# Optimization experiments

Measured on AMD Instinct MI355X. Metric: run time of the kernel, lower is better.

The kernel has to match this reference:

```python
import jax, jax.numpy as jnp
import numpy as np
from jax import lax

SCORE_THRESH = 0.05
NMS_THRESH = 0.5
DET_PER_IMG = 100
WX, WY, WW, WH = 10.0, 10.0, 5.0, 5.0   # BoxCoder weights
BBOX_XFORM_CLIP = float(np.log(1000.0 / 16.0))
NEG = -1e9  # sentinel for invalid / suppressed scores


def setup_inputs() -> dict:
    key = jax.random.key(0)
    k1, k2, k3 = jax.random.split(key, 3)
    R, C = 1000, 81
    W, H = 1333, 800
    class_logits = jax.random.normal(k1, (R, C), dtype=jnp.float32)
    box_regression = jax.random.normal(k2, (R, C * 4), dtype=jnp.float32)
    # build valid xyxy proposal boxes inside the image from uniform noise
    u = jax.random.uniform(k3, (R, 4), dtype=jnp.float32)
    x1 = u[:, 0] * (W - 120)
    y1 = u[:, 1] * (H - 120)
    x2 = jnp.minimum(x1 + 20.0 + u[:, 2] * 300.0, W - 1)
    y2 = jnp.minimum(y1 + 20.0 + u[:, 3] * 300.0, H - 1)
    proposals = jnp.stack([x1, y1, x2, y2], axis=1)
    return {"class_logits": class_logits, "box_regression": box_regression,
            "proposals": proposals, "image_w": W, "image_h": H}


def _decode(rel, boxes):
    """BoxCoder.decode: rel [R, C*4], boxes [R,4] xyxy -> [R, C, 4]."""
    w = boxes[:, 2] - boxes[:, 0] + 1.0
    h = boxes[:, 3] - boxes[:, 1] + 1.0
    cx = boxes[:, 0] + 0.5 * w
    cy = boxes[:, 1] + 0.5 * h
    dx = rel[:, 0::4] / WX
    dy = rel[:, 1::4] / WY
    dw = jnp.minimum(rel[:, 2::4] / WW, BBOX_XFORM_CLIP)
    dh = jnp.minimum(rel[:, 3::4] / WH, BBOX_XFORM_CLIP)
    pcx = dx * w[:, None] + cx[:, None]
    pcy = dy * h[:, None] + cy[:, None]
    pw = jnp.exp(dw) * w[:, None]
    ph = jnp.exp(dh) * h[:, None]
    return jnp.stack([pcx - 0.5 * pw, pcy - 0.5 * ph,
                      pcx + 0.5 * pw - 1.0, pcy + 0.5 * ph - 1.0], axis=-1)


def _pairwise_iou(b):
    """Legacy (+1) IoU: b [N,4] -> [N,N]."""
    area = (b[:, 2] - b[:, 0] + 1.0) * (b[:, 3] - b[:, 1] + 1.0)
    lt = jnp.maximum(b[:, None, :2], b[None, :, :2])
    rb = jnp.minimum(b[:, None, 2:], b[None, :, 2:])
    wh = jnp.clip(rb - lt + 1.0, 0.0)
    inter = wh[..., 0] * wh[..., 1]
    return inter / (area[:, None] + area[None, :] - inter)


def _nms_one_class(boxes, scores):
    """Greedy NMS for one class, fixed shape. Returns keep mask [N] in original order."""
    N = scores.shape[0]
    valid = scores > SCORE_THRESH
    order = jnp.argsort(-jnp.where(valid, scores, NEG))
    b = boxes[order]
    v = valid[order]
    iou = _pairwise_iou(b)  # [N,N], descending-score order
    idx = jnp.arange(N)

    def body(keep, xs):
        i, row, vi = xs
        suppressed = jnp.any(keep & (row > NMS_THRESH) & (idx < i))
        keep = keep.at[i].set(vi & jnp.logical_not(suppressed))
        return keep, None

    keep_sorted, _ = lax.scan(body, jnp.zeros(N, bool), (idx, iou, v))
    return jnp.zeros(N, bool).at[order].set(keep_sorted)


def _forward(class_logits, box_regression, proposals, image_w, image_h):
    probs = jax.nn.softmax(class_logits, axis=-1)          # [R, C]
    boxes = _decode(box_regression, proposals)             # [R, C, 4]
    # clip_to_image (remove_empty=False), legacy -1 convention
    x = jnp.clip(boxes[..., 0::2], 0.0, image_w - 1)
    y = jnp.clip(boxes[..., 1::2], 0.0, image_h - 1)
    boxes = jnp.stack([x[..., 0], y[..., 0], x[..., 1], y[..., 1]], axis=-1)
    # drop background class 0
    sc = probs[:, 1:].T                                    # [C-1, R]
    bc = jnp.transpose(boxes[:, 1:, :], (1, 0, 2))         # [C-1, R, 4]
    keep = jax.vmap(_nms_one_class)(bc, sc)                # [C-1, R]
    flat_s = jnp.where(keep, sc, NEG).reshape(-1)
    top_s, top_i = lax.top_k(flat_s, DET_PER_IMG)
    top_b = bc.reshape(-1, 4)[top_i]
    labels = top_i // sc.shape[1] + 1
    return top_s, top_b, labels


def reference(class_logits, box_regression, proposals, image_w, image_h):
    return _forward(class_logits, box_regression, proposals, image_w, image_h)
```

## Files before the change

kernel.cpp:

```cpp
#include <hip/hip_runtime.h>
#include <cmath>

#define R_ROWS 1000
#define NCLS   81
#define REGW   (NCLS * 4)
#define SCORE_T 0.05f
#define NMS_T   0.5f
#define NEG_S  -1e9f
#define DETS   100
#define CLIP_V 4.135166556742356f
#define MAXC   1000
#define SLOTS  1000
#define NBLK_CLS 80

#define NBINS    1024
#define CK_CAP   2560
#define SURV_CAP 512


__device__ __forceinline__ float4 decode_clip(const float* __restrict__ prop,
                                              const float* __restrict__ reg,
                                              int r, int ccol, float wmax, float hmax) {
    float x1 = prop[r * 4 + 0], y1 = prop[r * 4 + 1];
    float x2 = prop[r * 4 + 2], y2 = prop[r * 4 + 3];
    float w  = __fadd_rn(__fsub_rn(x2, x1), 1.0f);
    float h  = __fadd_rn(__fsub_rn(y2, y1), 1.0f);
    float cx = __fadd_rn(x1, __fmul_rn(0.5f, w));
    float cy = __fadd_rn(y1, __fmul_rn(0.5f, h));
    const float* rr = reg + r * REGW + 4 * ccol;
    float dx = rr[0] / 10.0f;
    float dy = rr[1] / 10.0f;
    float dw = fminf(rr[2] / 5.0f, CLIP_V);
    float dh = fminf(rr[3] / 5.0f, CLIP_V);
    float pcx = __fadd_rn(__fmul_rn(dx, w), cx);
    float pcy = __fadd_rn(__fmul_rn(dy, h), cy);
    float pw  = __fmul_rn(expf(dw), w);
    float ph  = __fmul_rn(expf(dh), h);
    float ox1 = __fsub_rn(pcx, __fmul_rn(0.5f, pw));
    float oy1 = __fsub_rn(pcy, __fmul_rn(0.5f, ph));
    float ox2 = __fsub_rn(__fadd_rn(pcx, __fmul_rn(0.5f, pw)), 1.0f);
    float oy2 = __fsub_rn(__fadd_rn(pcy, __fmul_rn(0.5f, ph)), 1.0f);
    float4 o;
    o.x = fminf(fmaxf(ox1, 0.0f), wmax);
    o.y = fminf(fmaxf(oy1, 0.0f), hmax);
    o.z = fminf(fmaxf(ox2, 0.0f), wmax);
    o.w = fminf(fmaxf(oy2, 0.0f), hmax);
    return o;
}

__device__ __forceinline__ float iou_legacy(float ax1, float ay1, float ax2, float ay2,
                                            float bx1, float by1, float bx2, float by2) {
    float aw = __fadd_rn(__fsub_rn(ax2, ax1), 1.0f);
    float ah = __fadd_rn(__fsub_rn(ay2, ay1), 1.0f);
    float areaA = __fmul_rn(aw, ah);
    float bw = __fadd_rn(__fsub_rn(bx2, bx1), 1.0f);
    float bh = __fadd_rn(__fsub_rn(by2, by1), 1.0f);
    float areaB = __fmul_rn(bw, bh);
    float ltx = fmaxf(ax1, bx1), lty = fmaxf(ay1, by1);
    float rbx = fminf(ax2, bx2), rby = fminf(ay2, by2);
    float wx = fmaxf(__fadd_rn(__fsub_rn(rbx, ltx), 1.0f), 0.0f);
    float wy = fmaxf(__fadd_rn(__fsub_rn(rby, lty), 1.0f), 0.0f);
    float inter = __fmul_rn(wx, wy);
    float denom = __fsub_rn(__fadd_rn(areaA, areaB), inter);
    return inter / denom;
}

__device__ __forceinline__ int bin_of(float s) {
    int idx = (int)(__float_as_uint(s) >> 16) - 0x3D00;
    return idx < 0 ? 0 : (idx > NBINS - 1 ? NBINS - 1 : idx);
}

__device__ __forceinline__ unsigned long long key_of(float s, unsigned f) {
    return ((unsigned long long)__float_as_uint(s) << 32) | (unsigned long long)(~f);
}
__device__ __forceinline__ float key_score(unsigned long long k) {
    return __uint_as_float((unsigned)(k >> 32));
}
__device__ __forceinline__ int key_flat(unsigned long long k) {
    return (int)(~(unsigned)k);
}

__device__ __forceinline__ void dev_store_u64(unsigned long long* p, unsigned long long v) {
    __hip_atomic_store(p, v, __ATOMIC_RELAXED, __HIP_MEMORY_SCOPE_AGENT);
}
__device__ __forceinline__ unsigned long long dev_load_u64(const unsigned long long* p) {
    return __hip_atomic_load(p, __ATOMIC_RELAXED, __HIP_MEMORY_SCOPE_AGENT);
}
__device__ __forceinline__ void dev_store_i32(int* p, int v) {
    __hip_atomic_store(p, v, __ATOMIC_RELAXED, __HIP_MEMORY_SCOPE_AGENT);
}

__device__ __forceinline__ int find_class(const int* koff, int g) {
    int lo = 0, hi = NBLK_CLS;
    while (hi - lo > 1) { int mid = (lo + hi) >> 1; if (g >= koff[mid]) lo = mid; else hi = mid; }
    return lo;
}


__global__ __launch_bounds__(64) void k_softmax_stats(const float* __restrict__ logits,
                                                      float* __restrict__ rowmax,
                                                      float* __restrict__ rowsum,
                                                      int* __restrict__ done) {
    int r = blockIdx.x;
    int l = threadIdx.x;
    if (r == 0 && l == 0) *done = 0;
    float v1 = logits[r * NCLS + l];
    float v2 = (l < NCLS - 64) ? logits[r * NCLS + 64 + l] : -INFINITY;
    float m = fmaxf(v1, v2);
    #pragma unroll
    for (int off = 32; off; off >>= 1) m = fmaxf(m, __shfl_xor(m, off));
    float s = expf(__fsub_rn(v1, m));
    if (l < NCLS - 64) s = __fadd_rn(s, expf(__fsub_rn(v2, m)));
    #pragma unroll
    for (int off = 32; off; off >>= 1) s = __fadd_rn(s, __shfl_xor(s, off));
    if (l == 0) { rowmax[r] = m; rowsum[r] = s; }
}


__global__ __launch_bounds__(256) void k_nms_select(const float* __restrict__ logits,
                                                    const float* __restrict__ reg,
                                                    const float* __restrict__ prop,
                                                    const float* __restrict__ rowmax,
                                                    const float* __restrict__ rowsum,
                                                    const int* __restrict__ piw,
                                                    const int* __restrict__ pih,
                                                    unsigned long long* __restrict__ klist,
                                                    int* __restrict__ kcount,
                                                    int* __restrict__ done,
                                                    float* __restrict__ out) {
    __shared__ float us[MAXC];  __shared__ int uidx[MAXC];
    __shared__ float ss[MAXC];  __shared__ int sidx[MAXC];
    __shared__ float bx4[MAXC][4];
    __shared__ int   supp[MAXC];
    __shared__ int   cnt, sh_last;
    __shared__ int   koff[NBLK_CLS + 1];
    __shared__ int   cs[256];
    __shared__ int   hist_s[NBINS];
    __shared__ unsigned long long ck[CK_CAP + 4];
    __shared__ unsigned long long cks[SURV_CAP + 4];
    __shared__ float sel_s[DETS]; __shared__ int sel_f[DETS];
    __shared__ int   sh_cut, sh_mcnt;

    const int cidx = blockIdx.x;
    const int ccol = cidx + 1;
    const int t    = threadIdx.x;
    const int lane = t & 63;
    const int wv   = t >> 6;
    const float wmax = (float)(*piw - 1);
    const float hmax = (float)(*pih - 1);

    if (t == 0) cnt = 0;
    __syncthreads();

    for (int r = t; r < R_ROWS; r += 256) {
        float z = logits[r * NCLS + ccol];
        float s = expf(__fsub_rn(z, rowmax[r])) / rowsum[r];
        if (s > SCORE_T) {
            int p = atomicAdd(&cnt, 1);
            us[p] = s; uidx[p] = r;
        }
    }
    __syncthreads();
    const int M = cnt;

    for (int i = t; i < M; i += 256) {
        float si = us[i]; int ri = uidx[i];
        int rank = 0;
        for (int j = 0; j < M; j++) {
            float sj = us[j]; int rj = uidx[j];
            rank += (sj > si) || (sj == si && rj < ri);
        }
        ss[rank] = si; sidx[rank] = ri;
    }
    __syncthreads();
    for (int i = t; i < M; i += 256) {
        float4 b = decode_clip(prop, reg, sidx[i], ccol, wmax, hmax);
        bx4[i][0] = b.x; bx4[i][1] = b.y; bx4[i][2] = b.z; bx4[i][3] = b.w;
        supp[i] = 0;
    }
    __syncthreads();

    if (M <= 64) {
        if (wv == 0) {
            const bool valid = lane < M;
            float b0 = 0, b1 = 0, b2 = 0, b3 = 0, sc = 0; int ri = 0;
            if (valid) { b0 = bx4[lane][0]; b1 = bx4[lane][1]; b2 = bx4[lane][2]; b3 = bx4[lane][3];
                         sc = ss[lane]; ri = sidx[lane]; }
            unsigned long long suppm = 0;
            for (int i = 0; i < M; ++i) {
                if ((suppm >> i) & 1ULL) continue;
                float ax1 = __shfl(b0, i), ay1 = __shfl(b1, i);
                float ax2 = __shfl(b2, i), ay2 = __shfl(b3, i);
                bool kill = valid && (lane > i) &&
                            (iou_legacy(ax1, ay1, ax2, ay2, b0, b1, b2, b3) > NMS_T);
                suppm |= __ballot(kill);
            }
            unsigned long long keepm = ~suppm;
            if (M < 64) keepm &= (1ULL << M) - 1ULL;
            if (valid && ((keepm >> lane) & 1ULL)) {
                int pos = __popcll(keepm & ((1ULL << lane) - 1ULL));
                dev_store_u64(&klist[(size_t)cidx * SLOTS + pos],
                              key_of(sc, (unsigned)(cidx * R_ROWS + ri)));
            }
            if (lane == 0) dev_store_i32(&kcount[cidx], __popcll(keepm));
        }
    } else {
        for (int i = 0; i < M; i++) {
            if (!supp[i]) {
                float ax1 = bx4[i][0], ay1 = bx4[i][1], ax2 = bx4[i][2], ay2 = bx4[i][3];
                for (int j = i + 1 + t; j < M; j += 256) {
                    if (!supp[j]) {
                        float v = iou_legacy(ax1, ay1, ax2, ay2,
                                             bx4[j][0], bx4[j][1], bx4[j][2], bx4[j][3]);
                        if (v > NMS_T) supp[j] = 1;
                    }
                }
            }
            __syncthreads();
        }
        for (int i = t; i < M; i += 256) {
            if (!supp[i]) {
                int pos = 0;
                for (int j = 0; j < i; ++j) pos += !supp[j];
                dev_store_u64(&klist[(size_t)cidx * SLOTS + pos],
                              key_of(ss[i], (unsigned)(cidx * R_ROWS + sidx[i])));
            }
        }
        if (t == 0) {
            int kc = 0;
            for (int i = 0; i < M; ++i) kc += !supp[i];
            dev_store_i32(&kcount[cidx], kc);
        }
    }

    __syncthreads();
    if (t == 0) sh_last = (atomicAdd(done, 1) == NBLK_CLS - 1) ? 1 : 0;
    __syncthreads();
    if (!sh_last) return;

    if (t < NBLK_CLS) cs[t] = atomicAdd(&kcount[t], 0);
    for (int b = t; b < NBINS; b += 256) hist_s[b] = 0;
    __syncthreads();
    if (t == 0) {
        int acc = 0;
        for (int c = 0; c < NBLK_CLS; ++c) { koff[c] = acc; acc += cs[c]; }
        koff[NBLK_CLS] = acc;
        sh_cut = 0; sh_mcnt = 0;
    }
    __syncthreads();
    const int K = koff[NBLK_CLS];
    const int target = (K < DETS) ? K : DETS;

    if (K <= CK_CAP) {
        for (int g = t; g < K; g += 256) {
            int c = find_class(koff, g);
            unsigned long long k = dev_load_u64(&klist[(size_t)c * SLOTS + (g - koff[c])]);
            ck[g] = k;
            atomicAdd(&hist_s[bin_of(key_score(k))], 1);
        }
        __syncthreads();

        int v0 = hist_s[4 * t], v1 = hist_s[4 * t + 1], v2 = hist_s[4 * t + 2], v3 = hist_s[4 * t + 3];
        int s3 = v3, s2 = v2 + s3, s1 = v1 + s2, s0 = v0 + s1;
        cs[t] = s0;
        __syncthreads();
        for (int off = 1; off < 256; off <<= 1) {
            int x = cs[t] + ((t + off < 256) ? cs[t + off] : 0);
            __syncthreads();
            cs[t] = x;
            __syncthreads();
        }
        int tail = (t < 255) ? cs[t + 1] : 0;
        int S0 = s0 + tail, S1 = s1 + tail, S2 = s2 + tail, S3 = s3 + tail;
        if (target > 0) {
            int best = -1;
            if      (S3 >= target) best = 4 * t + 3;
            else if (S2 >= target) best = 4 * t + 2;
            else if (S1 >= target) best = 4 * t + 1;
            else if (S0 >= target) best = 4 * t;
            if (best >= 0) atomicMax(&sh_cut, best);
        }
        __syncthreads();
        const int cut = sh_cut;

        for (int g = t; g < K; g += 256) {
            unsigned long long k = ck[g];
            if (bin_of(key_score(k)) >= cut) {
                int p = atomicAdd(&sh_mcnt, 1);
                if (p < SURV_CAP) cks[p] = k;
            }
        }
        __syncthreads();
        const int Mc = sh_mcnt;

        if (Mc <= SURV_CAP) {
            int Mp = (Mc + 3) & ~3;
            if (t < Mp - Mc) cks[Mc + t] = 0;
            __syncthreads();
            for (int i = t; i < Mc; i += 256) {
                unsigned long long ki = cks[i];
                int r = 0;
                for (int j = 0; j < Mp; j += 4)
                    r += (int)(cks[j] > ki) + (int)(cks[j + 1] > ki)
                       + (int)(cks[j + 2] > ki) + (int)(cks[j + 3] > ki);
                if (r < DETS) {
                    sel_s[r] = key_score(ki);
                    sel_f[r] = key_flat(ki);
                }
            }
        } else {
            int Kp = (K + 3) & ~3;
            if (t < Kp - K) ck[K + t] = 0;
            __syncthreads();
            for (int g = t; g < K; g += 256) {
                unsigned long long ki = ck[g];
                if (bin_of(key_score(ki)) < cut) continue;
                int r = 0;
                for (int j = 0; j < Kp; j += 4)
                    r += (int)(ck[j] > ki) + (int)(ck[j + 1] > ki)
                       + (int)(ck[j + 2] > ki) + (int)(ck[j + 3] > ki);
                if (r < DETS) {
                    sel_s[r] = key_score(ki);
                    sel_f[r] = key_flat(ki);
                }
            }
        }
    } else {
        for (int g = t; g < K; g += 256) {
            int c = find_class(koff, g);
            unsigned long long ki = dev_load_u64(&klist[(size_t)c * SLOTS + (g - koff[c])]);
            int r = 0;
            for (int g2 = 0; g2 < K; ++g2) {
                int c2 = find_class(koff, g2);
                r += (int)(dev_load_u64(&klist[(size_t)c2 * SLOTS + (g2 - koff[c2])]) > ki);
            }
            if (r < DETS) {
                sel_s[r] = key_score(ki);
                sel_f[r] = key_flat(ki);
            }
        }
    }
    __syncthreads();

    if (t == 0 && target < DETS) {
        int n = target, f = 0;
        while (n < DETS) {
            bool used = false;
            for (int q = 0; q < target; q++) if (key_flat(cks[q]) == f) { used = true; break; }
            if (!used) { sel_s[n] = NEG_S; sel_f[n] = f; n++; }
            f++;
        }
    }
    __syncthreads();

    if (t < DETS) {
        int f = sel_f[t];
        int c2 = f / R_ROWS;
        int r  = f % R_ROWS;
        float4 b = decode_clip(prop, reg, r, c2 + 1, wmax, hmax);
        out[t] = sel_s[t];
        out[DETS + 4 * t + 0] = b.x;
        out[DETS + 4 * t + 1] = b.y;
        out[DETS + 4 * t + 2] = b.z;
        out[DETS + 4 * t + 3] = b.w;
        out[DETS * 5 + t] = (float)(c2 + 1);
    }
}


extern "C" void kernel_launch(void* const* d_in, const int* in_sizes, int n_in,
                              void* d_out, int out_size, void* d_ws, size_t ws_size,
                              hipStream_t stream) {
    (void)in_sizes; (void)n_in; (void)out_size; (void)ws_size;
    const float* logits = (const float*)d_in[0];
    const float* reg    = (const float*)d_in[1];
    const float* prop   = (const float*)d_in[2];
    const int*   piw    = (const int*)d_in[3];
    const int*   pih    = (const int*)d_in[4];
    float* out = (float*)d_out;

    char* ws = (char*)d_ws;
    int*   done    = (int*)(ws);
    int*   kcount  = (int*)(ws + 64);
    float* rowmax  = (float*)(ws + 1024);
    float* rowsum  = (float*)(ws + 5120);
    unsigned long long* klist = (unsigned long long*)(ws + 12288);

    k_softmax_stats<<<dim3(R_ROWS), dim3(64), 0, stream>>>(logits, rowmax, rowsum, done);
    k_nms_select<<<dim3(NBLK_CLS), dim3(256), 0, stream>>>(logits, reg, prop, rowmax, rowsum,
                                                           piw, pih, klist, kcount, done, out);
}
```

Baseline: 38.32 us.

## Fuse softmax stats into NMS kernel with chunked LDS logits staging

Removes the separate softmax-stats kernel. Each of the 80 class blocks now recomputes the row max and sum for all 1000 rows, staging the logits through shared memory in 128-row chunks. Shared buffers are overlaid in one union region to make room for the staging area, and the done flag is reset with a memset. This saves a kernel launch and the global round trip for the stats, but every block redundantly reads the full logits matrix and does a serial 81-element softmax per thread, using only 128 of its 256 threads.

```diff
diff --git a/kernel.cpp b/kernel.cpp
--- a/kernel.cpp
+++ b/kernel.cpp
@@ -12,6 +12,9 @@
 #define MAXC   1000
 #define SLOTS  1000
 #define NBLK_CLS 80
+
+#define CHUNK_R 128
+#define NCHUNK  8
 
 #define NBINS    1024
 #define CK_CAP   2560
@@ -97,49 +100,30 @@
 }
 
 
-__global__ __launch_bounds__(64) void k_softmax_stats(const float* __restrict__ logits,
-                                                      float* __restrict__ rowmax,
-                                                      float* __restrict__ rowsum,
-                                                      int* __restrict__ done) {
-    int r = blockIdx.x;
-    int l = threadIdx.x;
-    if (r == 0 && l == 0) *done = 0;
-    float v1 = logits[r * NCLS + l];
-    float v2 = (l < NCLS - 64) ? logits[r * NCLS + 64 + l] : -INFINITY;
-    float m = fmaxf(v1, v2);
-    #pragma unroll
-    for (int off = 32; off; off >>= 1) m = fmaxf(m, __shfl_xor(m, off));
-    float s = expf(__fsub_rn(v1, m));
-    if (l < NCLS - 64) s = __fadd_rn(s, expf(__fsub_rn(v2, m)));
-    #pragma unroll
-    for (int off = 32; off; off >>= 1) s = __fadd_rn(s, __shfl_xor(s, off));
-    if (l == 0) { rowmax[r] = m; rowsum[r] = s; }
-}
-
-
-__global__ __launch_bounds__(256) void k_nms_select(const float* __restrict__ logits,
-                                                    const float* __restrict__ reg,
-                                                    const float* __restrict__ prop,
-                                                    const float* __restrict__ rowmax,
-                                                    const float* __restrict__ rowsum,
-                                                    const int* __restrict__ piw,
-                                                    const int* __restrict__ pih,
-                                                    unsigned long long* __restrict__ klist,
-                                                    int* __restrict__ kcount,
-                                                    int* __restrict__ done,
-                                                    float* __restrict__ out) {
+__global__ __launch_bounds__(256) void k_all(const float* __restrict__ logits,
+                                             const float* __restrict__ reg,
+                                             const float* __restrict__ prop,
+                                             const int* __restrict__ piw,
+                                             const int* __restrict__ pih,
+                                             unsigned long long* __restrict__ klist,
+                                             int* __restrict__ kcount,
+                                             int* __restrict__ done,
+                                             float* __restrict__ out) {
     __shared__ float us[MAXC];  __shared__ int uidx[MAXC];
-    __shared__ float ss[MAXC];  __shared__ int sidx[MAXC];
-    __shared__ float bx4[MAXC][4];
-    __shared__ int   supp[MAXC];
-    __shared__ int   cnt, sh_last;
+    __shared__ int cnt, sh_last;
     __shared__ int   koff[NBLK_CLS + 1];
     __shared__ int   cs[256];
-    __shared__ int   hist_s[NBINS];
-    __shared__ unsigned long long ck[CK_CAP + 4];
-    __shared__ unsigned long long cks[SURV_CAP + 4];
     __shared__ float sel_s[DETS]; __shared__ int sel_f[DETS];
     __shared__ int   sh_cut, sh_mcnt;
+    __shared__ __align__(16) char ubuf[41472];
+    float* chunkf = (float*)ubuf;
+    float* ss   = (float*)ubuf;
+    int*   sidx = (int*)(ubuf + 4000);
+    float (*bx4)[4] = (float(*)[4])(ubuf + 8000);
+    int*   supp = (int*)(ubuf + 24000);
+    int*   hist_s = (int*)ubuf;
+    unsigned long long* ck  = (unsigned long long*)(ubuf + 4096);
+    unsigned long long* cks = (unsigned long long*)(ubuf + 4096 + 8 * CK_CAP);
 
     const int cidx = blockIdx.x;
     const int ccol = cidx + 1;
@@ -152,15 +136,30 @@
     if (t == 0) cnt = 0;
     __syncthreads();
 
-    for (int r = t; r < R_ROWS; r += 256) {
-        float z = logits[r * NCLS + ccol];
-        float s = expf(__fsub_rn(z, rowmax[r])) / rowsum[r];
-        if (s > SCORE_T) {
-            int p = atomicAdd(&cnt, 1);
-            us[p] = s; uidx[p] = r;
-        }
-    }
-    __syncthreads();
+    for (int c = 0; c < NCHUNK; ++c) {
+        const int rb = c * CHUNK_R;
+        int n = R_ROWS - rb; if (n > CHUNK_R) n = CHUNK_R;
+        const int nw = n * NCLS;
+        const float4* src = (const float4*)(logits + rb * NCLS);
+        float4* dst = (float4*)chunkf;
+        for (int i = t; i < (nw >> 2); i += 256) dst[i] = src[i];
+        __syncthreads();
+        if (t < n) {
+            const float* row = chunkf + t * NCLS;
+            float m = row[0];
+            #pragma unroll 8
+            for (int k = 1; k < NCLS; ++k) m = fmaxf(m, row[k]);
+            float s = 0.0f;
+            #pragma unroll 8
+            for (int k = 0; k < NCLS; ++k) s = __fadd_rn(s, expf(__fsub_rn(row[k], m)));
+            float sc = expf(__fsub_rn(row[ccol], m)) / s;
+            if (sc > SCORE_T) {
+                int p = atomicAdd(&cnt, 1);
+                us[p] = sc; uidx[p] = rb + t;
+            }
+        }
+        __syncthreads();
+    }
     const int M = cnt;
 
     for (int i = t; i < M; i += 256) {
@@ -382,11 +381,9 @@
     char* ws = (char*)d_ws;
     int*   done    = (int*)(ws);
     int*   kcount  = (int*)(ws + 64);
-    float* rowmax  = (float*)(ws + 1024);
-    float* rowsum  = (float*)(ws + 5120);
-    unsigned long long* klist = (unsigned long long*)(ws + 12288);
-
-    k_softmax_stats<<<dim3(R_ROWS), dim3(64), 0, stream>>>(logits, rowmax, rowsum, done);
-    k_nms_select<<<dim3(NBLK_CLS), dim3(256), 0, stream>>>(logits, reg, prop, rowmax, rowsum,
-                                                           piw, pih, klist, kcount, done, out);
-}
+    unsigned long long* klist = (unsigned long long*)(ws + 4096);
+
+    hipMemsetAsync(ws, 0, 4, stream);
+    k_all<<<dim3(NBLK_CLS), dim3(256), 0, stream>>>(logits, reg, prop, piw, pih,
+                                                    klist, kcount, done, out);
+}
```

Result: slower. 102.5 us (+167.4%).

## Split last-block-done selection into a separate single-block kernel launch

Applied to the files above, without the earlier changes.

The per-class NMS kernel no longer uses an atomic done counter to elect a final block for global top-k selection. Selection now runs in its own one-block kernel, with the kernel boundary providing ordering, so plain loads and stores replace the agent-scope atomics. This shrinks the NMS kernel's shared memory, which may raise occupancy, and removes the atomic handoff. In exchange it adds a third kernel launch and its launch gap to the critical path.

```diff
diff --git a/kernel.cpp b/kernel.cpp
--- a/kernel.cpp
+++ b/kernel.cpp
@@ -80,16 +80,6 @@
     return (int)(~(unsigned)k);
 }
 
-__device__ __forceinline__ void dev_store_u64(unsigned long long* p, unsigned long long v) {
-    __hip_atomic_store(p, v, __ATOMIC_RELAXED, __HIP_MEMORY_SCOPE_AGENT);
-}
-__device__ __forceinline__ unsigned long long dev_load_u64(const unsigned long long* p) {
-    return __hip_atomic_load(p, __ATOMIC_RELAXED, __HIP_MEMORY_SCOPE_AGENT);
-}
-__device__ __forceinline__ void dev_store_i32(int* p, int v) {
-    __hip_atomic_store(p, v, __ATOMIC_RELAXED, __HIP_MEMORY_SCOPE_AGENT);
-}
-
 __device__ __forceinline__ int find_class(const int* koff, int g) {
     int lo = 0, hi = NBLK_CLS;
     while (hi - lo > 1) { int mid = (lo + hi) >> 1; if (g >= koff[mid]) lo = mid; else hi = mid; }
@@ -97,13 +87,11 @@
 }
 
 
-__global__ __launch_bounds__(64) void k_softmax_stats(const float* __restrict__ logits,
-                                                      float* __restrict__ rowmax,
-                                                      float* __restrict__ rowsum,
-                                                      int* __restrict__ done) {
+__global__ __launch_bounds__(64) void k_stats(const float* __restrict__ logits,
+                                              float* __restrict__ rowmax,
+                                              float* __restrict__ rowsum) {
     int r = blockIdx.x;
     int l = threadIdx.x;
-    if (r == 0 && l == 0) *done = 0;
     float v1 = logits[r * NCLS + l];
     float v2 = (l < NCLS - 64) ? logits[r * NCLS + 64 + l] : -INFINITY;
     float m = fmaxf(v1, v2);
@@ -117,29 +105,20 @@
 }
 
 
-__global__ __launch_bounds__(256) void k_nms_select(const float* __restrict__ logits,
-                                                    const float* __restrict__ reg,
-                                                    const float* __restrict__ prop,
-                                                    const float* __restrict__ rowmax,
-                                                    const float* __restrict__ rowsum,
-                                                    const int* __restrict__ piw,
-                                                    const int* __restrict__ pih,
-                                                    unsigned long long* __restrict__ klist,
-                                                    int* __restrict__ kcount,
-                                                    int* __restrict__ done,
-                                                    float* __restrict__ out) {
+__global__ __launch_bounds__(256) void k_nms(const float* __restrict__ logits,
+                                             const float* __restrict__ reg,
+                                             const float* __restrict__ prop,
+                                             const float* __restrict__ rowmax,
+                                             const float* __restrict__ rowsum,
+                                             const int* __restrict__ piw,
+                                             const int* __restrict__ pih,
+                                             unsigned long long* __restrict__ klist,
+                                             int* __restrict__ kcount) {
     __shared__ float us[MAXC];  __shared__ int uidx[MAXC];
     __shared__ float ss[MAXC];  __shared__ int sidx[MAXC];
     __shared__ float bx4[MAXC][4];
     __shared__ int   supp[MAXC];
-    __shared__ int   cnt, sh_last;
-    __shared__ int   koff[NBLK_CLS + 1];
-    __shared__ int   cs[256];
-    __shared__ int   hist_s[NBINS];
-    __shared__ unsigned long long ck[CK_CAP + 4];
-    __shared__ unsigned long long cks[SURV_CAP + 4];
-    __shared__ float sel_s[DETS]; __shared__ int sel_f[DETS];
-    __shared__ int   sh_cut, sh_mcnt;
+    __shared__ int   cnt;
 
     const int cidx = blockIdx.x;
     const int ccol = cidx + 1;
@@ -199,10 +178,9 @@
             if (M < 64) keepm &= (1ULL << M) - 1ULL;
             if (valid && ((keepm >> lane) & 1ULL)) {
                 int pos = __popcll(keepm & ((1ULL << lane) - 1ULL));
-                dev_store_u64(&klist[(size_t)cidx * SLOTS + pos],
-                              key_of(sc, (unsigned)(cidx * R_ROWS + ri)));
-            }
-            if (lane == 0) dev_store_i32(&kcount[cidx], __popcll(keepm));
+                klist[(size_t)cidx * SLOTS + pos] = key_of(sc, (unsigned)(cidx * R_ROWS + ri));
+            }
+            if (lane == 0) kcount[cidx] = __popcll(keepm);
         }
     } else {
         for (int i = 0; i < M; i++) {
@@ -222,23 +200,38 @@
             if (!supp[i]) {
                 int pos = 0;
                 for (int j = 0; j < i; ++j) pos += !supp[j];
-                dev_store_u64(&klist[(size_t)cidx * SLOTS + pos],
-                              key_of(ss[i], (unsigned)(cidx * R_ROWS + sidx[i])));
+                klist[(size_t)cidx * SLOTS + pos] = key_of(ss[i], (unsigned)(cidx * R_ROWS + sidx[i]));
             }
         }
         if (t == 0) {
             int kc = 0;
             for (int i = 0; i < M; ++i) kc += !supp[i];
-            dev_store_i32(&kcount[cidx], kc);
-        }
-    }
-
-    __syncthreads();
-    if (t == 0) sh_last = (atomicAdd(done, 1) == NBLK_CLS - 1) ? 1 : 0;
-    __syncthreads();
-    if (!sh_last) return;
-
-    if (t < NBLK_CLS) cs[t] = atomicAdd(&kcount[t], 0);
+            kcount[cidx] = kc;
+        }
+    }
+}
+
+
+__global__ __launch_bounds__(256) void k_select(const float* __restrict__ reg,
+                                                const float* __restrict__ prop,
+                                                const int* __restrict__ piw,
+                                                const int* __restrict__ pih,
+                                                const unsigned long long* __restrict__ klist,
+                                                const int* __restrict__ kcount,
+                                                float* __restrict__ out) {
+    __shared__ int   koff[NBLK_CLS + 1];
+    __shared__ int   cs[256];
+    __shared__ int   hist_s[NBINS];
+    __shared__ unsigned long long ck[CK_CAP + 4];
+    __shared__ unsigned long long cks[SURV_CAP + 4];
+    __shared__ float sel_s[DETS]; __shared__ int sel_f[DETS];
+    __shared__ int   sh_cut, sh_mcnt;
+
+    const int t = threadIdx.x;
+    const float wmax = (float)(*piw - 1);
+    const float hmax = (float)(*pih - 1);
+
+    if (t < NBLK_CLS) cs[t] = kcount[t];
     for (int b = t; b < NBINS; b += 256) hist_s[b] = 0;
     __syncthreads();
     if (t == 0) {
@@ -254,7 +247,7 @@
     if (K <= CK_CAP) {
         for (int g = t; g < K; g += 256) {
             int c = find_class(koff, g);
-            unsigned long long k = dev_load_u64(&klist[(size_t)c * SLOTS + (g - koff[c])]);
+            unsigned long long k = klist[(size_t)c * SLOTS + (g - koff[c])];
             ck[g] = k;
             atomicAdd(&hist_s[bin_of(key_score(k))], 1);
         }
@@ -328,11 +321,11 @@
     } else {
         for (int g = t; g < K; g += 256) {
             int c = find_class(koff, g);
-            unsigned long long ki = dev_load_u64(&klist[(size_t)c * SLOTS + (g - koff[c])]);
+            unsigned long long ki = klist[(size_t)c * SLOTS + (g - koff[c])];
             int r = 0;
             for (int g2 = 0; g2 < K; ++g2) {
                 int c2 = find_class(koff, g2);
-                r += (int)(dev_load_u64(&klist[(size_t)c2 * SLOTS + (g2 - koff[c2])]) > ki);
+                r += (int)(klist[(size_t)c2 * SLOTS + (g2 - koff[c2])] > ki);
             }
             if (r < DETS) {
                 sel_s[r] = key_score(ki);
@@ -380,13 +373,13 @@
     float* out = (float*)d_out;
 
     char* ws = (char*)d_ws;
-    int*   done    = (int*)(ws);
-    int*   kcount  = (int*)(ws + 64);
+    int*   kcount  = (int*)(ws);
     float* rowmax  = (float*)(ws + 1024);
     float* rowsum  = (float*)(ws + 5120);
     unsigned long long* klist = (unsigned long long*)(ws + 12288);
 
-    k_softmax_stats<<<dim3(R_ROWS), dim3(64), 0, stream>>>(logits, rowmax, rowsum, done);
-    k_nms_select<<<dim3(NBLK_CLS), dim3(256), 0, stream>>>(logits, reg, prop, rowmax, rowsum,
-                                                           piw, pih, klist, kcount, done, out);
-}
+    k_stats<<<dim3(R_ROWS), dim3(64), 0, stream>>>(logits, rowmax, rowsum);
+    k_nms<<<dim3(NBLK_CLS), dim3(256), 0, stream>>>(logits, reg, prop, rowmax, rowsum,
+                                                    piw, pih, klist, kcount);
+    k_select<<<dim3(1), dim3(256), 0, stream>>>(reg, prop, piw, pih, klist, kcount, out);
+}
```

After: 38.83 us. No clear change (+1.3%).

## Emit thresholded score keys in softmax kernel; NMS reads compacted per-class lists

Applied to the files above, without the earlier changes.

The softmax stats kernel now computes the per-class probabilities itself and appends packed (score, index) keys above threshold into per-class global lists via atomics. The NMS kernel no longer rescans all 1000 logits per class; it loads the compacted list and ranks with single 64-bit key compares. A memset is added to zero the counters, and the emit order is nondeterministic, which the full-key rank sort makes harmless. This trades a redundant per-class pass for global atomics and an extra memset launch.

```diff
diff --git a/kernel.cpp b/kernel.cpp
--- a/kernel.cpp
+++ b/kernel.cpp
@@ -9,13 +9,14 @@
 #define NEG_S  -1e9f
 #define DETS   100
 #define CLIP_V 4.135166556742356f
-#define MAXC   1000
 #define SLOTS  1000
 #define NBLK_CLS 80
 
 #define NBINS    1024
 #define CK_CAP   2560
 #define SURV_CAP 512
+
+typedef unsigned long long ull;
 
 
 __device__ __forceinline__ float4 decode_clip(const float* __restrict__ prop,
@@ -70,20 +71,16 @@
     return idx < 0 ? 0 : (idx > NBINS - 1 ? NBINS - 1 : idx);
 }
 
-__device__ __forceinline__ unsigned long long key_of(float s, unsigned f) {
-    return ((unsigned long long)__float_as_uint(s) << 32) | (unsigned long long)(~f);
-}
-__device__ __forceinline__ float key_score(unsigned long long k) {
-    return __uint_as_float((unsigned)(k >> 32));
-}
-__device__ __forceinline__ int key_flat(unsigned long long k) {
-    return (int)(~(unsigned)k);
-}
-
-__device__ __forceinline__ void dev_store_u64(unsigned long long* p, unsigned long long v) {
+__device__ __forceinline__ ull key_of(float s, unsigned f) {
+    return ((ull)__float_as_uint(s) << 32) | (ull)(~f);
+}
+__device__ __forceinline__ float key_score(ull k) { return __uint_as_float((unsigned)(k >> 32)); }
+__device__ __forceinline__ int   key_flat(ull k)  { return (int)(~(unsigned)k); }
+
+__device__ __forceinline__ void dev_store_u64(ull* p, ull v) {
     __hip_atomic_store(p, v, __ATOMIC_RELAXED, __HIP_MEMORY_SCOPE_AGENT);
 }
-__device__ __forceinline__ unsigned long long dev_load_u64(const unsigned long long* p) {
+__device__ __forceinline__ ull dev_load_u64(const ull* p) {
     return __hip_atomic_load(p, __ATOMIC_RELAXED, __HIP_MEMORY_SCOPE_AGENT);
 }
 __device__ __forceinline__ void dev_store_i32(int* p, int v) {
@@ -97,13 +94,11 @@
 }
 
 
-__global__ __launch_bounds__(64) void k_softmax_stats(const float* __restrict__ logits,
-                                                      float* __restrict__ rowmax,
-                                                      float* __restrict__ rowsum,
-                                                      int* __restrict__ done) {
+__global__ __launch_bounds__(64) void k_stats_emit(const float* __restrict__ logits,
+                                                   int* __restrict__ cnt,
+                                                   ull* __restrict__ klistA) {
     int r = blockIdx.x;
     int l = threadIdx.x;
-    if (r == 0 && l == 0) *done = 0;
     float v1 = logits[r * NCLS + l];
     float v2 = (l < NCLS - 64) ? logits[r * NCLS + 64 + l] : -INFINITY;
     float m = fmaxf(v1, v2);
@@ -113,31 +108,45 @@
     if (l < NCLS - 64) s = __fadd_rn(s, expf(__fsub_rn(v2, m)));
     #pragma unroll
     for (int off = 32; off; off >>= 1) s = __fadd_rn(s, __shfl_xor(s, off));
-    if (l == 0) { rowmax[r] = m; rowsum[r] = s; }
-}
-
-
-__global__ __launch_bounds__(256) void k_nms_select(const float* __restrict__ logits,
-                                                    const float* __restrict__ reg,
+
+    if (l >= 1) {
+        float sc = expf(__fsub_rn(v1, m)) / s;
+        if (sc > SCORE_T) {
+            int p = atomicAdd(&cnt[l], 1);
+            klistA[(size_t)(l - 1) * SLOTS + p] = key_of(sc, (unsigned)((l - 1) * R_ROWS + r));
+        }
+    }
+    if (l < NCLS - 64) {
+        int c = 64 + l;
+        float sc = expf(__fsub_rn(v2, m)) / s;
+        if (sc > SCORE_T) {
+            int p = atomicAdd(&cnt[c], 1);
+            klistA[(size_t)(c - 1) * SLOTS + p] = key_of(sc, (unsigned)((c - 1) * R_ROWS + r));
+        }
+    }
+}
+
+
+__global__ __launch_bounds__(256) void k_nms_select(const float* __restrict__ reg,
                                                     const float* __restrict__ prop,
-                                                    const float* __restrict__ rowmax,
-                                                    const float* __restrict__ rowsum,
                                                     const int* __restrict__ piw,
                                                     const int* __restrict__ pih,
-                                                    unsigned long long* __restrict__ klist,
+                                                    const int* __restrict__ cnt,
+                                                    const ull* __restrict__ klistA,
+                                                    ull* __restrict__ klistB,
                                                     int* __restrict__ kcount,
                                                     int* __restrict__ done,
                                                     float* __restrict__ out) {
-    __shared__ float us[MAXC];  __shared__ int uidx[MAXC];
-    __shared__ float ss[MAXC];  __shared__ int sidx[MAXC];
-    __shared__ float bx4[MAXC][4];
-    __shared__ int   supp[MAXC];
-    __shared__ int   cnt, sh_last;
+    __shared__ ull ku[SLOTS];
+    __shared__ ull ks[SLOTS];
+    __shared__ float bx4[SLOTS][4];
+    __shared__ int   supp[SLOTS];
+    __shared__ int   sh_last;
     __shared__ int   koff[NBLK_CLS + 1];
     __shared__ int   cs[256];
     __shared__ int   hist_s[NBINS];
-    __shared__ unsigned long long ck[CK_CAP + 4];
-    __shared__ unsigned long long cks[SURV_CAP + 4];
+    __shared__ ull   ck[CK_CAP + 4];
+    __shared__ ull   cks[SURV_CAP + 4];
     __shared__ float sel_s[DETS]; __shared__ int sel_f[DETS];
     __shared__ int   sh_cut, sh_mcnt;
 
@@ -149,32 +158,22 @@
     const float wmax = (float)(*piw - 1);
     const float hmax = (float)(*pih - 1);
 
-    if (t == 0) cnt = 0;
-    __syncthreads();
-
-    for (int r = t; r < R_ROWS; r += 256) {
-        float z = logits[r * NCLS + ccol];
-        float s = expf(__fsub_rn(z, rowmax[r])) / rowsum[r];
-        if (s > SCORE_T) {
-            int p = atomicAdd(&cnt, 1);
-            us[p] = s; uidx[p] = r;
-        }
-    }
-    __syncthreads();
-    const int M = cnt;
+    int M = cnt[ccol]; if (M > SLOTS) M = SLOTS;
+
+    for (int i = t; i < M; i += 256) ku[i] = klistA[(size_t)cidx * SLOTS + i];
+    __syncthreads();
 
     for (int i = t; i < M; i += 256) {
-        float si = us[i]; int ri = uidx[i];
+        ull ki = ku[i];
         int rank = 0;
-        for (int j = 0; j < M; j++) {
-            float sj = us[j]; int rj = uidx[j];
-            rank += (sj > si) || (sj == si && rj < ri);
-        }
-        ss[rank] = si; sidx[rank] = ri;
-    }
-    __syncthreads();
+        for (int j = 0; j < M; j++) rank += (int)(ku[j] > ki);
+        ks[rank] = ki;
+    }
+    __syncthreads();
+
     for (int i = t; i < M; i += 256) {
-        float4 b = decode_clip(prop, reg, sidx[i], ccol, wmax, hmax);
+        int row = key_flat(ks[i]) - cidx * R_ROWS;
+        float4 b = decode_clip(prop, reg, row, ccol, wmax, hmax);
         bx4[i][0] = b.x; bx4[i][1] = b.y; bx4[i][2] = b.z; bx4[i][3] = b.w;
         supp[i] = 0;
     }
@@ -183,10 +182,10 @@
     if (M <= 64) {
         if (wv == 0) {
             const bool valid = lane < M;
-            float b0 = 0, b1 = 0, b2 = 0, b3 = 0, sc = 0; int ri = 0;
+            float b0 = 0, b1 = 0, b2 = 0, b3 = 0; ull ke = 0;
             if (valid) { b0 = bx4[lane][0]; b1 = bx4[lane][1]; b2 = bx4[lane][2]; b3 = bx4[lane][3];
-                         sc = ss[lane]; ri = sidx[lane]; }
-            unsigned long long suppm = 0;
+                         ke = ks[lane]; }
+            ull suppm = 0;
             for (int i = 0; i < M; ++i) {
                 if ((suppm >> i) & 1ULL) continue;
                 float ax1 = __shfl(b0, i), ay1 = __shfl(b1, i);
@@ -195,12 +194,11 @@
                             (iou_legacy(ax1, ay1, ax2, ay2, b0, b1, b2, b3) > NMS_T);
                 suppm |= __ballot(kill);
             }
-            unsigned long long keepm = ~suppm;
+            ull keepm = ~suppm;
             if (M < 64) keepm &= (1ULL << M) - 1ULL;
             if (valid && ((keepm >> lane) & 1ULL)) {
                 int pos = __popcll(keepm & ((1ULL << lane) - 1ULL));
-                dev_store_u64(&klist[(size_t)cidx * SLOTS + pos],
-                              key_of(sc, (unsigned)(cidx * R_ROWS + ri)));
+                dev_store_u64(&klistB[(size_t)cidx * SLOTS + pos], ke);
             }
             if (lane == 0) dev_store_i32(&kcount[cidx], __popcll(keepm));
         }
@@ -222,8 +220,7 @@
             if (!supp[i]) {
                 int pos = 0;
                 for (int j = 0; j < i; ++j) pos += !supp[j];
-                dev_store_u64(&klist[(size_t)cidx * SLOTS + pos],
-                              key_of(ss[i], (unsigned)(cidx * R_ROWS + sidx[i])));
+                dev_store_u64(&klistB[(size_t)cidx * SLOTS + pos], ks[i]);
             }
         }
         if (t == 0) {
@@ -254,7 +251,7 @@
     if (K <= CK_CAP) {
         for (int g = t; g < K; g += 256) {
             int c = find_class(koff, g);
-            unsigned long long k = dev_load_u64(&klist[(size_t)c * SLOTS + (g - koff[c])]);
+            ull k = dev_load_u64(&klistB[(size_t)c * SLOTS + (g - koff[c])]);
             ck[g] = k;
             atomicAdd(&hist_s[bin_of(key_score(k))], 1);
         }
@@ -284,7 +281,7 @@
         const int cut = sh_cut;
 
         for (int g = t; g < K; g += 256) {
-            unsigned long long k = ck[g];
+            ull k = ck[g];
             if (bin_of(key_score(k)) >= cut) {
                 int p = atomicAdd(&sh_mcnt, 1);
                 if (p < SURV_CAP) cks[p] = k;
@@ -298,46 +295,37 @@
             if (t < Mp - Mc) cks[Mc + t] = 0;
             __syncthreads();
             for (int i = t; i < Mc; i += 256) {
-                unsigned long long ki = cks[i];
+                ull ki = cks[i];
                 int r = 0;
                 for (int j = 0; j < Mp; j += 4)
                     r += (int)(cks[j] > ki) + (int)(cks[j + 1] > ki)
                        + (int)(cks[j + 2] > ki) + (int)(cks[j + 3] > ki);
-                if (r < DETS) {
-                    sel_s[r] = key_score(ki);
-                    sel_f[r] = key_flat(ki);
-                }
+                if (r < DETS) { sel_s[r] = key_score(ki); sel_f[r] = key_flat(ki); }
             }
         } else {
             int Kp = (K + 3) & ~3;
             if (t < Kp - K) ck[K + t] = 0;
             __syncthreads();
             for (int g = t; g < K; g += 256) {
-                unsigned long long ki = ck[g];
+                ull ki = ck[g];
                 if (bin_of(key_score(ki)) < cut) continue;
                 int r = 0;
                 for (int j = 0; j < Kp; j += 4)
                     r += (int)(ck[j] > ki) + (int)(ck[j + 1] > ki)
                        + (int)(ck[j + 2] > ki) + (int)(ck[j + 3] > ki);
-                if (r < DETS) {
-                    sel_s[r] = key_score(ki);
-                    sel_f[r] = key_flat(ki);
-                }
+                if (r < DETS) { sel_s[r] = key_score(ki); sel_f[r] = key_flat(ki); }
             }
         }
     } else {
         for (int g = t; g < K; g += 256) {
             int c = find_class(koff, g);
-            unsigned long long ki = dev_load_u64(&klist[(size_t)c * SLOTS + (g - koff[c])]);
+            ull ki = dev_load_u64(&klistB[(size_t)c * SLOTS + (g - koff[c])]);
             int r = 0;
             for (int g2 = 0; g2 < K; ++g2) {
                 int c2 = find_class(koff, g2);
-                r += (int)(dev_load_u64(&klist[(size_t)c2 * SLOTS + (g2 - koff[c2])]) > ki);
-            }
-            if (r < DETS) {
-                sel_s[r] = key_score(ki);
-                sel_f[r] = key_flat(ki);
-            }
+                r += (int)(dev_load_u64(&klistB[(size_t)c2 * SLOTS + (g2 - koff[c2])]) > ki);
+            }
+            if (r < DETS) { sel_s[r] = key_score(ki); sel_f[r] = key_flat(ki); }
         }
     }
     __syncthreads();
@@ -380,13 +368,15 @@
     float* out = (float*)d_out;
 
     char* ws = (char*)d_ws;
-    int*   done    = (int*)(ws);
-    int*   kcount  = (int*)(ws + 64);
-    float* rowmax  = (float*)(ws + 1024);
-    float* rowsum  = (float*)(ws + 5120);
-    unsigned long long* klist = (unsigned long long*)(ws + 12288);
-
-    k_softmax_stats<<<dim3(R_ROWS), dim3(64), 0, stream>>>(logits, rowmax, rowsum, done);
-    k_nms_select<<<dim3(NBLK_CLS), dim3(256), 0, stream>>>(logits, reg, prop, rowmax, rowsum,
-                                                           piw, pih, klist, kcount, done, out);
-}
+    int* done   = (int*)(ws);
+    int* cnt    = (int*)(ws + 64);
+    int* kcount = (int*)(ws + 1024);
+    ull* klistA = (ull*)(ws + 4096);
+    ull* klistB = (ull*)(ws + 4096 + (size_t)NBLK_CLS * SLOTS * 8);
+
+    hipMemsetAsync(ws, 0, 512, stream);
+    k_stats_emit<<<dim3(R_ROWS), dim3(64), 0, stream>>>(logits, cnt, klistA);
+    k_nms_select<<<dim3(NBLK_CLS), dim3(256), 0, stream>>>(reg, prop, piw, pih,
+                                                           cnt, klistA, klistB,
+                                                           kcount, done, out);
+}
```

New measurement: 42.99 us. 12.2% more time.
